# Optimization experiments

Hardware: AMD Instinct MI355X
Metric: run time of the kernel (lower is better)

## Reference

```python
import jax, jax.numpy as jnp
import numpy as np

E = 1024  # embed_dim
H = 16    # num_heads
D = E // H  # head_dim
B, S = 2, 2048


def setup_inputs() -> dict:
    key = jax.random.key(0)
    ks = jax.random.split(key, 8)
    q = jax.random.normal(ks[0], (B, S, E), dtype=jnp.float32)
    k = jax.random.normal(ks[1], (B, S, E), dtype=jnp.float32)
    v = jax.random.normal(ks[2], (B, S, E), dtype=jnp.float32)
    mask = jax.random.randint(ks[3], (1, 1, S, S), 0, 2, dtype=jnp.int32)
    sc = 1.0 / np.sqrt(E)
    Wqkv = jax.random.normal(ks[4], (E, 3 * E), dtype=jnp.float32) * sc  # [in, out]
    bqkv = jnp.zeros((3 * E,), dtype=jnp.float32)
    Wout = jax.random.normal(ks[5], (E, E), dtype=jnp.float32) * sc
    bout = jnp.zeros((E,), dtype=jnp.float32)
    return {"q": q, "k": k, "v": v, "mask": mask,
            "Wqkv": Wqkv, "bqkv": bqkv, "Wout": Wout, "bout": bout}


def reference(q, k, v, mask, Wqkv, bqkv, Wout, bout):
    # Fused QKV projection: project cat([q,k,v], dim=0) with the shared 3E proj,
    # then take the Q slice for q, K slice for k, V slice for v.
    x = jnp.concatenate([q, k, v], axis=0)            # [3B, S, E]
    full = jnp.einsum('bse,ef->bsf', x, Wqkv) + bqkv  # [3B, S, 3E]
    qf, kf, vf = jnp.split(full, 3, axis=0)           # each [B, S, 3E]
    qh = qf[..., :E].reshape(B, S, H, D).transpose(0, 2, 1, 3)       # [B,H,S,D]
    kh = kf[..., E:2 * E].reshape(B, S, H, D).transpose(0, 2, 1, 3)
    vh = vf[..., 2 * E:].reshape(B, S, H, D).transpose(0, 2, 1, 3)
    scores = jnp.einsum('bhqd,bhkd->bhqk', qh, kh) / np.sqrt(D)      # [B,H,S,S]
    scores = jnp.where(mask == 0, -jnp.inf, scores)
    attn = jax.nn.softmax(scores, axis=-1)
    ctx = jnp.einsum('bhqk,bhkd->bhqd', attn, vh)                    # [B,H,S,D]
    ctx = ctx.transpose(0, 2, 1, 3).reshape(B, S, E)
    return jnp.einsum('bse,ef->bsf', ctx, Wout) + bout
```

## Files before the change

### kernel.cpp

```cpp
#include <hip/hip_runtime.h>
#include <stdint.h>

#define EDIM 1024
#define HNUM 16
#define HD   64
#define BB   2
#define SS   2048
#define MTOT (BB * SS)

typedef __attribute__((ext_vector_type(8))) __bf16 bf16x8;
typedef __attribute__((ext_vector_type(8))) short short8;
typedef __attribute__((ext_vector_type(4))) short short4v;
typedef __attribute__((ext_vector_type(4))) float f32x4;
typedef __attribute__((ext_vector_type(16))) float f32x16;

__device__ __forceinline__ short bfbits(float f) {
  __bf16 h = (__bf16)f;
  return __builtin_bit_cast(short, h);
}

__device__ __forceinline__ void gload16(const void* g, void* l) {
  __builtin_amdgcn_global_load_lds((const __attribute__((address_space(1))) void*)g,
                                   (__attribute__((address_space(3))) void*)l, 16, 0, 0);
}

__device__ __forceinline__ int sigma_perm(int k) {
  return (k & ~0xC) | ((k & 4) << 1) | ((k & 8) >> 1);
}

__global__ __launch_bounds__(256) void prep(
    const float* __restrict__ q, const float* __restrict__ k,
    const float* __restrict__ v, const float* __restrict__ Wqkv,
    const float* __restrict__ Wout, const int* __restrict__ mask,
    short* __restrict__ Qb, short* __restrict__ Kb, short* __restrict__ Vb,
    short* __restrict__ WqT, short* __restrict__ WkT, short* __restrict__ WvT,
    short* __restrict__ WoT, unsigned long long* __restrict__ pm) {
  __shared__ short L[64][80];
  const int bid = blockIdx.x, t = threadIdx.x;

  if (bid < 6144) {
    const int which = bid >> 11;
    const int i = (bid & 2047) * 256 + t;
    const float* s = which == 0 ? q : (which == 1 ? k : v);
    short* d = which == 0 ? Qb : (which == 1 ? Kb : Vb);
    const float4* sp = (const float4*)s + (size_t)i * 2;
    float4 a = sp[0], b = sp[1];
    short8 r;
    r[0] = bfbits(a.x); r[1] = bfbits(a.y); r[2] = bfbits(a.z); r[3] = bfbits(a.w);
    r[4] = bfbits(b.x); r[5] = bfbits(b.y); r[6] = bfbits(b.z); r[7] = bfbits(b.w);
    *(short8*)(d + (size_t)i * 8) = r;
  } else if (bid < 7168) {
    const int tb = bid - 6144;
    const int which = tb >> 8;
    const int k0 = ((tb >> 4) & 15) * 64, n0 = (tb & 15) * 64;
    const float* W = which == 3 ? Wout : Wqkv;
    const int ld = which == 3 ? EDIM : 3 * EDIM;
    const int col0 = which == 3 ? 0 : which * EDIM;
    short* D = which == 0 ? WqT : (which == 1 ? WkT : (which == 2 ? WvT : WoT));
    {
      const int kr = t >> 2, nc0 = (t & 3) * 16;
      #pragma unroll
      for (int u = 0; u < 4; ++u) {
        float4 f = *(const float4*)(W + (size_t)(k0 + kr) * ld + col0 + n0 + nc0 + u * 4);
        L[nc0 + u * 4 + 0][kr] = bfbits(f.x);
        L[nc0 + u * 4 + 1][kr] = bfbits(f.y);
        L[nc0 + u * 4 + 2][kr] = bfbits(f.z);
        L[nc0 + u * 4 + 3][kr] = bfbits(f.w);
      }
    }
    __syncthreads();
    {
      const int nr = t >> 2, kc = (t & 3) * 16;
      #pragma unroll
      for (int u = 0; u < 2; ++u) {
        short8 vv = *(const short8*)&L[nr][kc + u * 8];
        *(short8*)(D + (size_t)(n0 + nr) * EDIM + k0 + kc + u * 8) = vv;
      }
    }
  } else {
    const int wid = (bid - 7168) * 4 + (t >> 6);
    const int lane = t & 63;
    const int qq = wid >> 5, kt = wid & 31;
    const int m = mask[(size_t)qq * SS + kt * 64 + lane];
    const unsigned long long b = __ballot(m != 0);
    if (lane == 0) pm[(size_t)qq * 32 + kt] = b;
  }
}

template <int NFR, int MODE, typename OT>
__device__ __forceinline__ void gemm_body(
    const short* __restrict__ A, const short* __restrict__ Bt,
    const float* __restrict__ bias, OT* __restrict__ O,
    int m0, int n0, int K, int N, float scale, short* As, short* Bs) {
  const int t = threadIdx.x;
  const int w = t >> 6, l = t & 63;
  const int wr = w >> 1, wc = w & 1;
  const int lr4 = l >> 4, lc = l & 15;

  f32x4 acc[4][NFR] = {};
  const int srow = t >> 3;
  const int schunk = (t & 7) ^ (srow & 7);

  for (int k0 = 0; k0 < K; k0 += 64) {
    #pragma unroll
    for (int p = 0; p < 4; ++p)
      gload16(A + (size_t)(m0 + 32 * p + srow) * K + k0 + schunk * 8,
              As + p * 2048 + w * 512);
    #pragma unroll
    for (int p = 0; p < NFR; ++p)
      gload16(Bt + (size_t)(n0 + 32 * p + srow) * K + k0 + schunk * 8,
              Bs + p * 2048 + w * 512);
    __syncthreads();

    #pragma unroll
    for (int kf = 0; kf < 2; ++kf) {
      const int c = ((4 * kf + lr4) ^ (lc & 7)) * 8;
      bf16x8 a[4], bfr[NFR];
      #pragma unroll
      for (int i = 0; i < 4; ++i)
        a[i] = *(const bf16x8*)(As + (64 * wr + 16 * i + lc) * 64 + c);
      #pragma unroll
      for (int j = 0; j < NFR; ++j)
        bfr[j] = *(const bf16x8*)(Bs + (16 * NFR * wc + 16 * j + lc) * 64 + c);
      #pragma unroll
      for (int i = 0; i < 4; ++i)
        #pragma unroll
        for (int j = 0; j < NFR; ++j)
          acc[i][j] = __builtin_amdgcn_mfma_f32_16x16x32_bf16(a[i], bfr[j], acc[i][j], 0, 0, 0);
    }
    __syncthreads();
  }

  #pragma unroll
  for (int j = 0; j < NFR; ++j) {
    const int col = n0 + 16 * NFR * wc + 16 * j + lc;
    const float bv = bias[col];
    #pragma unroll
    for (int i = 0; i < 4; ++i) {
      const int rbase = m0 + 64 * wr + 16 * i + 4 * lr4;
      if constexpr (MODE == 2) {
        const int bidx = rbase >> 11, s = rbase & 2047;
        const int hh = col >> 6, dd = col & 63;
        short4v o;
        #pragma unroll
        for (int r = 0; r < 4; ++r) o[r] = bfbits((acc[i][j][r] + bv) * scale);
        *(short4v*)((short*)O + (((size_t)bidx * HNUM + hh) * 64 + dd) * SS +
                    (s & ~63) + sigma_perm(s & 63)) = o;
      } else {
        #pragma unroll
        for (int r = 0; r < 4; ++r) {
          float vv = (acc[i][j][r] + bv) * scale;
          if constexpr (MODE == 0)
            ((short*)O)[(size_t)(rbase + r) * N + col] = bfbits(vv);
          else
            ((float*)O)[(size_t)(rbase + r) * N + col] = vv;
        }
      }
    }
  }
}

__global__ __launch_bounds__(256) void gemm_qkv(
    const short* __restrict__ Qb, const short* __restrict__ Kb,
    const short* __restrict__ Vb, const short* __restrict__ WqT,
    const short* __restrict__ WkT, const short* __restrict__ WvT,
    const float* __restrict__ bqkv, short* __restrict__ Qpj,
    short* __restrict__ Kpj, short* __restrict__ VT) {
  __shared__ short As[128 * 64];
  __shared__ short Bs[128 * 64];
  const int sel = blockIdx.y >> 3;
  const int n0 = (blockIdx.y & 7) * 128;
  const int m0 = blockIdx.x * 128;
  if (sel == 0)
    gemm_body<4, 0, short>(Qb, WqT, bqkv, Qpj, m0, n0, EDIM, EDIM,
                           0.125f * 1.44269504089f, As, Bs);
  else if (sel == 1)
    gemm_body<4, 0, short>(Kb, WkT, bqkv + EDIM, Kpj, m0, n0, EDIM, EDIM,
                           1.0f, As, Bs);
  else
    gemm_body<4, 2, short>(Vb, WvT, bqkv + 2 * EDIM, VT, m0, n0, EDIM, EDIM,
                           1.0f, As, Bs);
}

__global__ __launch_bounds__(256) void gemm_out(
    const short* __restrict__ A, const short* __restrict__ Bt,
    const float* __restrict__ bias, float* __restrict__ O) {
  __shared__ short As[128 * 64];
  __shared__ short Bs[64 * 64];
  gemm_body<2, 1, float>(A, Bt, bias, O, blockIdx.x * 128, blockIdx.y * 64,
                         EDIM, EDIM, 1.0f, As, Bs);
}

__global__ __launch_bounds__(128) void attn_mfma(
    const short* __restrict__ Qp, const short* __restrict__ Kp,
    const short* __restrict__ VT, const unsigned long long* __restrict__ pmask,
    short* __restrict__ Ctx) {
  __shared__ short Ks[2][4096];
  __shared__ short Vt[2][4096];

  const int t = threadIdx.x, w = t >> 6, l = t & 63;
  const int l31 = l & 31, h32 = l >> 5;
  const int q0 = blockIdx.x * 64;
  const int h = blockIdx.y, b = blockIdx.z;
  const size_t hb = (size_t)b * SS * EDIM + (size_t)h * HD;
  const size_t hv = ((size_t)b * HNUM + h) * (size_t)64 * SS;
  const int qrow = q0 + 32 * w + l31;

  bf16x8 qf[4];
  #pragma unroll
  for (int c = 0; c < 4; ++c)
    qf[c] = *(const bf16x8*)(Qp + hb + (size_t)qrow * EDIM + 16 * c + 8 * h32);

  int roff[4];
  #pragma unroll
  for (int c = 0; c < 4; ++c) roff[c] = ((2 * c + h32) ^ (l & 7)) * 8;
  const int rowb = l31 * 64;

  const int sr = l >> 3;
  const int sc = (l & 7) ^ sr;
  const short* ksrc = Kp + hb + (size_t)(32 * w + sr) * EDIM + sc * 8;
  const short* vsrc = VT + hv + (size_t)(32 * w + sr) * SS + sc * 8;
  const int ldst = w * 2048;

  #pragma unroll
  for (int p = 0; p < 4; ++p) {
    gload16(ksrc + (size_t)(8 * p) * EDIM, &Ks[0][ldst + p * 512]);
    gload16(vsrc + (size_t)(8 * p) * SS,  &Vt[0][ldst + p * 512]);
  }
  ksrc += (size_t)64 * EDIM;
  vsrc += 64;
  __syncthreads();

  f32x16 accO[2] = {};
  float mrow = -1e30f, lrow = 0.f;
  const unsigned long long* pmp = pmask + (size_t)qrow * (SS / 64);
  const int NT = SS / 64;

  for (int kt = 0; kt < NT; ++kt) {
    const int cur = kt & 1, nxt = cur ^ 1;
    const unsigned long long pw = pmp[kt];
    if (kt + 1 < NT) {
      #pragma unroll
      for (int p = 0; p < 4; ++p) {
        gload16(ksrc + (size_t)(8 * p) * EDIM, &Ks[nxt][ldst + p * 512]);
        gload16(vsrc + (size_t)(8 * p) * SS,  &Vt[nxt][ldst + p * 512]);
      }
      ksrc += (size_t)64 * EDIM;
      vsrc += 64;
    }

    f32x16 sacc[2] = {};
    #pragma unroll
    for (int c = 0; c < 4; ++c) {
      bf16x8 ka = *(const bf16x8*)(&Ks[cur][rowb + roff[c]]);
      bf16x8 kb = *(const bf16x8*)(&Ks[cur][2048 + rowb + roff[c]]);
      sacc[0] = __builtin_amdgcn_mfma_f32_32x32x16_bf16(ka, qf[c], sacc[0], 0, 0, 0);
      sacc[1] = __builtin_amdgcn_mfma_f32_32x32x16_bf16(kb, qf[c], sacc[1], 0, 0, 0);
    }

    float mA = -1e30f, mB = -1e30f;
    #pragma unroll
    for (int T = 0; T < 2; ++T)
      #pragma unroll
      for (int g = 0; g < 4; ++g) {
        mA = fmaxf(mA, fmaxf(sacc[T][4 * g + 0], sacc[T][4 * g + 1]));
        mB = fmaxf(mB, fmaxf(sacc[T][4 * g + 2], sacc[T][4 * g + 3]));
      }
    float mt = fmaxf(mA, mB);
    mt = fmaxf(mt, __shfl_xor(mt, 32, 64));

    if (__any(mt > mrow + 7.0f)) {
      const float mn = fmaxf(mrow, mt);
      const float scl = exp2f(mrow - mn);
      mrow = mn;
      lrow *= scl;
      #pragma unroll
      for (int dt = 0; dt < 2; ++dt)
        #pragma unroll
        for (int r = 0; r < 16; ++r) accO[dt][r] *= scl;
    }

    const unsigned long long pwh = pw >> (4 * h32);
    float ls = 0.f;
    union { unsigned u[4]; bf16x8 v; } pk[4];
    #pragma unroll
    for (int kc = 0; kc < 4; ++kc) {
      const int T = kc >> 1, rb = 8 * (kc & 1);
      #pragma unroll
      for (int wd = 0; wd < 4; ++wd) {
        const int r0 = rb + 2 * wd, r1 = r0 + 1;
        const int bit0 = 32 * T + 8 * (r0 >> 2) + (r0 & 3);
        const int bit1 = 32 * T + 8 * (r1 >> 2) + (r1 & 3);
        const float e0 = exp2f(sacc[T][r0] - mrow);
        const float e1 = exp2f(sacc[T][r1] - mrow);
        const float p0 = ((pwh >> bit0) & 1ull) ? e0 : 0.f;
        const float p1 = ((pwh >> bit1) & 1ull) ? e1 : 0.f;
        ls += p0 + p1;
        const unsigned b0 = (unsigned short)__builtin_bit_cast(unsigned short, (__bf16)p0);
        const unsigned b1 = (unsigned short)__builtin_bit_cast(unsigned short, (__bf16)p1);
        pk[kc].u[wd] = b0 | (b1 << 16);
      }
    }
    ls += __shfl_xor(ls, 32, 64);
    lrow += ls;

    #pragma unroll
    for (int kc = 0; kc < 4; ++kc) {
      bf16x8 va = *(const bf16x8*)(&Vt[cur][rowb + roff[kc]]);
      bf16x8 vb = *(const bf16x8*)(&Vt[cur][2048 + rowb + roff[kc]]);
      accO[0] = __builtin_amdgcn_mfma_f32_32x32x16_bf16(va, pk[kc].v, accO[0], 0, 0, 0);
      accO[1] = __builtin_amdgcn_mfma_f32_32x32x16_bf16(vb, pk[kc].v, accO[1], 0, 0, 0);
    }
    __syncthreads();
  }

  const float inv = 1.f / lrow;
  #pragma unroll
  for (int dt = 0; dt < 2; ++dt)
    #pragma unroll
    for (int g = 0; g < 4; ++g) {
      short4v o;
      #pragma unroll
      for (int r = 0; r < 4; ++r) o[r] = bfbits(accO[dt][4 * g + r] * inv);
      *(short4v*)(Ctx + hb + (size_t)qrow * EDIM + 32 * dt + 8 * g + 4 * h32) = o;
    }
}

extern "C" void kernel_launch(void* const* d_in, const int* in_sizes, int n_in,
                              void* d_out, int out_size, void* d_ws, size_t ws_size,
                              hipStream_t stream) {
  const float* q    = (const float*)d_in[0];
  const float* k    = (const float*)d_in[1];
  const float* v    = (const float*)d_in[2];
  const int*   mask = (const int*)d_in[3];
  const float* Wqkv = (const float*)d_in[4];
  const float* bqkv = (const float*)d_in[5];
  const float* Wout = (const float*)d_in[6];
  const float* bout = (const float*)d_in[7];
  float* out = (float*)d_out;

  const size_t mat = (size_t)MTOT * EDIM;
  const size_t wmat = (size_t)EDIM * EDIM;
  short* Qb  = (short*)d_ws;
  short* Kb  = Qb + mat;
  short* Vb  = Kb + mat;
  short* WqT = Vb + mat;
  short* WkT = WqT + wmat;
  short* WvT = WkT + wmat;
  short* WoT = WvT + wmat;
  short* Qpj = WoT + wmat;
  short* Kpj = Qpj + mat;
  short* VT  = Kpj + mat;
  short* Ctx = VT + mat;
  unsigned long long* pm = (unsigned long long*)(Ctx + mat);

  prep<<<dim3(23552), 256, 0, stream>>>(q, k, v, Wqkv, Wout, mask,
                                        Qb, Kb, Vb, WqT, WkT, WvT, WoT, pm);

  gemm_qkv<<<dim3(MTOT / 128, 24), 256, 0, stream>>>(Qb, Kb, Vb, WqT, WkT, WvT,
                                                     bqkv, Qpj, Kpj, VT);

  attn_mfma<<<dim3(SS / 64, HNUM, BB), 128, 0, stream>>>(Qpj, Kpj, VT, pm, Ctx);

  gemm_out<<<dim3(MTOT / 128, EDIM / 64), 256, 0, stream>>>(Ctx, WoT, bout, out);
}
```

Before: 292.3 us.

## Widen attention blocks to 128 queries with remapped grid and stronger LDS swizzle

The attention kernel now runs 4 waves per block covering 128 query rows, so each K/V tile staged in LDS serves twice as many queries, and each thread issues half as many async loads. The 1D grid is remapped with an XCD-aware index permutation so blocks of the same head and batch land together for L2 reuse. The LDS swizzle gains an extra row-dependent XOR term to reduce bank conflicts, and s_setprio raises wave priority around the MFMA sections. Risks include fewer blocks in the grid (512) and possible occupancy or register pressure changes at 256 threads.

Result: faster. 280.7 us (-4.0%).

```diff
diff --git a/kernel.cpp b/kernel.cpp
--- a/kernel.cpp
+++ b/kernel.cpp
@@ -191,7 +191,7 @@
                          EDIM, EDIM, 1.0f, As, Bs);
 }
 
-__global__ __launch_bounds__(128) void attn_mfma(
+__global__ __launch_bounds__(256) void attn_mfma(
     const short* __restrict__ Qp, const short* __restrict__ Kp,
     const short* __restrict__ VT, const unsigned long long* __restrict__ pmask,
     short* __restrict__ Ctx) {
@@ -200,8 +200,9 @@
 
   const int t = threadIdx.x, w = t >> 6, l = t & 63;
   const int l31 = l & 31, h32 = l >> 5;
-  const int q0 = blockIdx.x * 64;
-  const int h = blockIdx.y, b = blockIdx.z;
+  const int lin = (blockIdx.x & 7) * 64 + (blockIdx.x >> 3);
+  const int qt = lin & 15, h = (lin >> 4) & 15, b = lin >> 8;
+  const int q0 = qt * 128;
   const size_t hb = (size_t)b * SS * EDIM + (size_t)h * HD;
   const size_t hv = ((size_t)b * HNUM + h) * (size_t)64 * SS;
   const int qrow = q0 + 32 * w + l31;
@@ -211,24 +212,28 @@
   for (int c = 0; c < 4; ++c)
     qf[c] = *(const bf16x8*)(Qp + hb + (size_t)qrow * EDIM + 16 * c + 8 * h32);
 
+  const int rswz = ((l31 >> 3) & 3) << 1;
   int roff[4];
   #pragma unroll
-  for (int c = 0; c < 4; ++c) roff[c] = ((2 * c + h32) ^ (l & 7)) * 8;
+  for (int c = 0; c < 4; ++c) roff[c] = (((2 * c + h32) ^ (l & 7) ^ rswz) * 8);
   const int rowb = l31 * 64;
 
-  const int sr = l >> 3;
-  const int sc = (l & 7) ^ sr;
-  const short* ksrc = Kp + hb + (size_t)(32 * w + sr) * EDIM + sc * 8;
-  const short* vsrc = VT + hv + (size_t)(32 * w + sr) * SS + sc * 8;
-  const int ldst = w * 2048;
-
-  #pragma unroll
-  for (int p = 0; p < 4; ++p) {
-    gload16(ksrc + (size_t)(8 * p) * EDIM, &Ks[0][ldst + p * 512]);
-    gload16(vsrc + (size_t)(8 * p) * SS,  &Vt[0][ldst + p * 512]);
-  }
-  ksrc += (size_t)64 * EDIM;
-  vsrc += 64;
+  const int sr8 = l >> 3;
+  const int g2a = 2 * w, g2b = 2 * w + 1;
+  const int sca = (l & 7) ^ sr8 ^ ((g2a & 3) << 1);
+  const int scb = (l & 7) ^ sr8 ^ ((g2b & 3) << 1);
+  const short* ksA = Kp + hb + (size_t)(8 * g2a + sr8) * EDIM + sca * 8;
+  const short* ksB = Kp + hb + (size_t)(8 * g2b + sr8) * EDIM + scb * 8;
+  const short* vsA = VT + hv + (size_t)(8 * g2a + sr8) * SS + sca * 8;
+  const short* vsB = VT + hv + (size_t)(8 * g2b + sr8) * SS + scb * 8;
+  const int ldA = g2a * 512, ldB = g2b * 512;
+
+  gload16(ksA, &Ks[0][ldA + l * 8]);
+  gload16(ksB, &Ks[0][ldB + l * 8]);
+  gload16(vsA, &Vt[0][ldA + l * 8]);
+  gload16(vsB, &Vt[0][ldB + l * 8]);
+  ksA += (size_t)64 * EDIM; ksB += (size_t)64 * EDIM;
+  vsA += 64; vsB += 64;
   __syncthreads();
 
   f32x16 accO[2] = {};
@@ -240,16 +245,16 @@
     const int cur = kt & 1, nxt = cur ^ 1;
     const unsigned long long pw = pmp[kt];
     if (kt + 1 < NT) {
-      #pragma unroll
-      for (int p = 0; p < 4; ++p) {
-        gload16(ksrc + (size_t)(8 * p) * EDIM, &Ks[nxt][ldst + p * 512]);
-        gload16(vsrc + (size_t)(8 * p) * SS,  &Vt[nxt][ldst + p * 512]);
-      }
-      ksrc += (size_t)64 * EDIM;
-      vsrc += 64;
+      gload16(ksA, &Ks[nxt][ldA + l * 8]);
+      gload16(ksB, &Ks[nxt][ldB + l * 8]);
+      gload16(vsA, &Vt[nxt][ldA + l * 8]);
+      gload16(vsB, &Vt[nxt][ldB + l * 8]);
+      ksA += (size_t)64 * EDIM; ksB += (size_t)64 * EDIM;
+      vsA += 64; vsB += 64;
     }
 
     f32x16 sacc[2] = {};
+    __builtin_amdgcn_s_setprio(1);
     #pragma unroll
     for (int c = 0; c < 4; ++c) {
       bf16x8 ka = *(const bf16x8*)(&Ks[cur][rowb + roff[c]]);
@@ -257,6 +262,7 @@
       sacc[0] = __builtin_amdgcn_mfma_f32_32x32x16_bf16(ka, qf[c], sacc[0], 0, 0, 0);
       sacc[1] = __builtin_amdgcn_mfma_f32_32x32x16_bf16(kb, qf[c], sacc[1], 0, 0, 0);
     }
+    __builtin_amdgcn_s_setprio(0);
 
     float mA = -1e30f, mB = -1e30f;
     #pragma unroll
@@ -304,6 +310,7 @@
     ls += __shfl_xor(ls, 32, 64);
     lrow += ls;
 
+    __builtin_amdgcn_s_setprio(1);
     #pragma unroll
     for (int kc = 0; kc < 4; ++kc) {
       bf16x8 va = *(const bf16x8*)(&Vt[cur][rowb + roff[kc]]);
@@ -311,6 +318,7 @@
       accO[0] = __builtin_amdgcn_mfma_f32_32x32x16_bf16(va, pk[kc].v, accO[0], 0, 0, 0);
       accO[1] = __builtin_amdgcn_mfma_f32_32x32x16_bf16(vb, pk[kc].v, accO[1], 0, 0, 0);
     }
+    __builtin_amdgcn_s_setprio(0);
     __syncthreads();
   }
 
@@ -360,7 +368,7 @@
   gemm_qkv<<<dim3(MTOT / 128, 24), 256, 0, stream>>>(Qb, Kb, Vb, WqT, WkT, WvT,
                                                      bqkv, Qpj, Kpj, VT);
 
-  attn_mfma<<<dim3(SS / 64, HNUM, BB), 128, 0, stream>>>(Qpj, Kpj, VT, pm, Ctx);
+  attn_mfma<<<dim3(512), 256, 0, stream>>>(Qpj, Kpj, VT, pm, Ctx);
 
   gemm_out<<<dim3(MTOT / 128, EDIM / 64), 256, 0, stream>>>(Ctx, WoT, bout, out);
 }
```
